# Performance work log

Measured on AMD Instinct MI355X. Metric: run time of the kernel, lower is better.

Reference implementation:

```python
import jax, jax.numpy as jnp
import numpy as np

N = 100000      # nodes
E = 1600000     # directed edges (bidirectional pairs)
DIN = 64
DOUT = 64
T = 3
LMBDA = 0.5
EPS = 1e-9


def setup_inputs() -> dict:
    key = jax.random.key(0)
    k1, k2, k3, k4 = jax.random.split(key, 4)
    x = jax.random.normal(k1, (N, DIN), dtype=jnp.float32)
    Eh = E // 2
    s = jax.random.randint(k2, (Eh,), 0, N)
    d = jax.random.randint(k3, (Eh,), 0, N)
    # bidirectional layout required by assert_bidirectional:
    # row0 = [s, d], row1 = [d, s]
    edge_index = jnp.stack([jnp.concatenate([s, d]), jnp.concatenate([d, s])]).astype(jnp.int32)
    W = jax.random.normal(k4, (DIN, DOUT), dtype=jnp.float32) / np.sqrt(DIN)
    b = jnp.zeros((DOUT,), dtype=jnp.float32)
    lmbda = jnp.float32(LMBDA)
    return {"x": x, "edge_index": edge_index, "W": W, "b": b, "lmbda": lmbda}


def _ema(h, src, dst, lmbda):
    # h: [N, D] node features after linear; src/dst: [E] int
    Eh = src.shape[0] // 2
    deg = jax.ops.segment_sum(jnp.ones(src.shape[0], h.dtype), src, num_segments=N)  # [N]
    h_e = h[src]                       # [E, D]  (expand)
    deg_e = deg[src][:, None]          # [E, 1]
    M = h_e                            # initial edge messages M_ij = x_i
    m = jax.ops.segment_sum(M, dst, num_segments=N)  # [N, D]  (aggregate)
    coef = lmbda / (deg_e - 1.0 + EPS)

    def step(carry, _):
        M, m = carry
        m_e = m[src]                                   # [E, D]
        M_ji = jnp.roll(M, -Eh, axis=0)                # reversed-edge messages
        M_new = jnp.where(deg_e == 1.0, h_e,
                          (1.0 - lmbda) * h_e + coef * (m_e - M_ji))
        m_new = jax.ops.segment_sum(M_new, dst, num_segments=N)
        return (M_new, m_new), None

    (M, m), _ = jax.lax.scan(step, (M, m), None, length=T)
    degN = deg[:, None]
    return jnp.where(degN == 0.0, h,
                     (1.0 - lmbda) * h + lmbda / (degN + EPS) * m)


def reference(x, edge_index, W, b, lmbda):
    src, dst = edge_index[0], edge_index[1]
    x_in = x                       # dim_in == dim_out -> residual uses pre-linear x
    h = x @ W + b                  # pyg_nn.Linear
    y = jax.nn.relu(_ema(h, src, dst, lmbda))
    # dropout p=0.0 (eval) is identity
    return x_in + y
```

## Files before the change

### kernel.cpp

```cpp
#include <hip/hip_runtime.h>
#include <hip/hip_bf16.h>


static __device__ __forceinline__ float bf2f(unsigned short v) {
    union { unsigned int u; float f; } x;
    x.u = ((unsigned int)v) << 16;
    return x.f;
}

static __device__ __forceinline__ unsigned short f2bf(float f) {
    union { unsigned int u; float f; } x;
    x.f = f;
    unsigned int r = x.u + 0x7FFFu + ((x.u >> 16) & 1u);
    return (unsigned short)(r >> 16);
}

static __device__ __forceinline__ float edge_c(int dm1) {
    float fd = (float)dm1;
    float raw = 0.5f * __builtin_amdgcn_rcpf(fd);
    return (fd == 0.0f) ? 0.0f : raw;
}

__global__ void ema_gemm_kernel(const float* __restrict__ x, const float* __restrict__ W,
                                const float* __restrict__ bias, unsigned short* __restrict__ hbf) {
    int wave = (int)((blockIdx.x * 256 + threadIdx.x) >> 6);
    int lane = (int)(threadIdx.x & 63);
    int n0 = wave * 8;
    if (n0 >= 100000) return;
    float w[64];
    #pragma unroll
    for (int k = 0; k < 64; ++k) w[k] = W[k * 64 + lane];
    float bv = bias[lane];
    int nend = (n0 + 8 < 100000) ? (n0 + 8) : 100000;
    for (int n = n0; n < nend; ++n) {
        const float* xr = x + (size_t)__builtin_amdgcn_readfirstlane(n) * 64;
        float acc = bv;
        #pragma unroll
        for (int k = 0; k < 64; ++k) acc = fmaf(xr[k], w[k], acc);
        hbf[n * 64 + lane] = f2bf(acc);
    }
}

__global__ void ema_hist_kernel(const int* ei, int* hcnt) {
    __shared__ int hist[391];
    int t = (int)threadIdx.x;
    int bl = (int)blockIdx.x;
    for (int i = t; i < 391; i += 256) hist[i] = 0;
    __syncthreads();
    int e0 = bl * 4096;
    #pragma unroll
    for (int i = 0; i < 16; ++i) {
        int e = e0 + t + i * 256;
        if (e < 1600000) {
            int dst = (e < 800000) ? ei[e + 800000] : ei[e - 800000];
            atomicAdd(&hist[dst >> 8], 1);
        }
    }
    __syncthreads();
    for (int i = t; i < 391; i += 256) hcnt[i * 391 + bl] = hist[i];
}

__global__ void ema_bscan_row_kernel(int* hcnt, int* btot) {
    __shared__ int s[512];
    int bu = (int)blockIdx.x;
    int t = (int)threadIdx.x;
    int v = (t < 391) ? hcnt[bu * 391 + t] : 0;
    s[t] = v;
    __syncthreads();
    for (int off = 1; off < 512; off <<= 1) {
        int add = (t >= off) ? s[t - off] : 0;
        __syncthreads();
        s[t] += add;
        __syncthreads();
    }
    if (t < 391) hcnt[bu * 391 + t] = s[t] - v;
    if (t == 390) btot[bu] = s[t];
}

__global__ void ema_bscan_base_kernel(const int* btot, int* bbase) {
    __shared__ int s[512];
    int t = (int)threadIdx.x;
    int v = (t < 391) ? btot[t] : 0;
    s[t] = v;
    __syncthreads();
    for (int off = 1; off < 512; off <<= 1) {
        int add = (t >= off) ? s[t - off] : 0;
        __syncthreads();
        s[t] += add;
        __syncthreads();
    }
    if (t < 391) bbase[t] = s[t] - v;
    if (t == 390) bbase[391] = s[t];
}

__global__ void ema_scatter_kernel(const int* ei, const int* hcnt,
                                   const int* bbase, unsigned int* stage) {
    __shared__ int base[391];
    __shared__ int cnt[391];
    int t = (int)threadIdx.x;
    int bl = (int)blockIdx.x;
    for (int i = t; i < 391; i += 256) {
        base[i] = hcnt[i * 391 + bl] + bbase[i];
        cnt[i] = 0;
    }
    __syncthreads();
    int e0 = bl * 4096;
    #pragma unroll
    for (int i = 0; i < 16; ++i) {
        int e = e0 + t + i * 256;
        if (e < 1600000) {
            int src = ei[e];
            int dst = (e < 800000) ? ei[e + 800000] : ei[e - 800000];
            int bu = dst >> 8;
            int slot = base[bu] + atomicAdd(&cnt[bu], 1);
            stage[slot] = ((unsigned int)(dst & 255) << 24) | (unsigned int)src;
        }
    }
}

__global__ void ema_fillcsr_count_kernel(const int* __restrict__ bbase,
                                         const unsigned int* __restrict__ stage,
                                         int* __restrict__ degi,
                                         int* __restrict__ rs) {
    __shared__ int cnt[256];
    __shared__ int scn[256];
    int b = (int)blockIdx.x;
    int t = (int)threadIdx.x;
    cnt[t] = 0;
    __syncthreads();
    int seg_lo = bbase[b];
    int seg_hi = bbase[b + 1];
    for (int i = seg_lo + t; i < seg_hi; i += 256) {
        atomicAdd(&cnt[stage[i] >> 24], 1);
    }
    __syncthreads();
    int v = cnt[t];
    scn[t] = v;
    __syncthreads();
    for (int off = 1; off < 256; off <<= 1) {
        int add = (t >= off) ? scn[t - off] : 0;
        __syncthreads();
        scn[t] += add;
        __syncthreads();
    }
    int node = (b << 8) + t;
    if (node < 100000) {
        degi[node] = v;
        rs[node] = seg_lo + scn[t] - v;
    }
}

__global__ void ema_fillcsr_write_kernel(const int* __restrict__ rs,
                                         const unsigned int* __restrict__ stage,
                                         const int* __restrict__ degi,
                                         int* __restrict__ csr,
                                         float* __restrict__ cf) {
    __shared__ int rsl[256];
    __shared__ int cnt[256];
    int b = (int)blockIdx.x;
    int t = (int)threadIdx.x;
    int node_lo = b << 8;
    int node = node_lo + t;
    rsl[t] = (node < 100000) ? rs[node] : 1600000;
    cnt[t] = 0;
    __syncthreads();
    int seg_lo = rsl[0];
    int seg_hi = (node_lo + 256 < 100000) ? rs[node_lo + 256] : 1600000;
    for (int i = seg_lo + t; i < seg_hi; i += 256) {
        unsigned int v = stage[i];
        int local = (int)(v >> 24);
        int srcn = (int)(v & 0x00FFFFFFu);
        int dm1 = degi[srcn] - 1;
        if (dm1 < 0) dm1 = 0;
        if (dm1 > 32767) dm1 = 32767;
        int slot = rsl[local] + atomicAdd(&cnt[local], 1);
        csr[slot] = (dm1 << 17) | srcn;
        cf[slot] = edge_c(dm1);
    }
}

__global__ void ema_cfcopy_kernel(const float4* __restrict__ cf4,
                                  float4* __restrict__ cfD4) {
    int i = (int)(blockIdx.x * 256 + threadIdx.x);
    if (i < 400000) cfD4[i] = cf4[i];
}

__global__ void ema_passA_kernel(const int* __restrict__ degi, const int* __restrict__ rs,
                                 const int* __restrict__ csr, const float* __restrict__ cf,
                                 const unsigned short* __restrict__ hbf,
                                 unsigned short* __restrict__ m0, unsigned short* __restrict__ W1,
                                 unsigned short* __restrict__ W2, unsigned short* __restrict__ W3a,
                                 float2* __restrict__ pp) {
    int wid = (int)((blockIdx.x * 256 + threadIdx.x) >> 6);
    int c = (int)(threadIdx.x & 63);
    if (wid >= 100000) return;
    int dv = __builtin_amdgcn_readfirstlane(degi[wid]);
    int base = wid * 64 + c;
    float hv = bf2f(hbf[base]);
    if (dv == 0) {
        m0[base] = 0;
        W1[base] = 0;
        W2[base] = 0;
        W3a[base] = f2bf(hv);
        if (c == 0) pp[wid] = make_float2(0.0f, 0.0f);
        return;
    }
    int j = __builtin_amdgcn_readfirstlane(rs[wid]);
    int end = j + dv;
    float av = (dv > 1) ? 0.5f : 1.0f;
    float cv = (dv > 1) ? 0.5f / ((float)dv - 1.0f + 1e-9f) : 0.0f;
    float fv = av * hv;
    float sm = 0.0f, sS = 0.0f, sQ = 0.0f, p1 = 0.0f, p2 = 0.0f;
    for (; j + 4 <= end; j += 4) {
        unsigned int w0 = (unsigned int)csr[j];
        unsigned int w1 = (unsigned int)csr[j + 1];
        unsigned int w2 = (unsigned int)csr[j + 2];
        unsigned int w3 = (unsigned int)csr[j + 3];
        int a0 = (int)(w0 & 0x1FFFFu), d0 = (int)(w0 >> 17);
        int a1 = (int)(w1 & 0x1FFFFu), d1 = (int)(w1 >> 17);
        int a2 = (int)(w2 & 0x1FFFFu), d2 = (int)(w2 >> 17);
        int a3 = (int)(w3 & 0x1FFFFu), d3 = (int)(w3 >> 17);
        float c0 = cf[j], c1 = cf[j + 1], c2 = cf[j + 2], c3 = cf[j + 3];
        float h0 = bf2f(hbf[a0 * 64 + c]);
        float h1 = bf2f(hbf[a1 * 64 + c]);
        float h2 = bf2f(hbf[a2 * 64 + c]);
        float h3 = bf2f(hbf[a3 * 64 + c]);
        float al0 = d0 ? 0.5f : 1.0f;
        float al1 = d1 ? 0.5f : 1.0f;
        float al2 = d2 ? 0.5f : 1.0f;
        float al3 = d3 ? 0.5f : 1.0f;
        sm += (h0 + h1) + (h2 + h3);
        sS += al0 * h0 + al1 * h1 + al2 * h2 + al3 * h3;
        sQ += c0 * h0 + c1 * h1 + c2 * h2 + c3 * h3;
        p1 += (c0 + c1) + (c2 + c3);
        p2 += c0 * c0 + c1 * c1 + c2 * c2 + c3 * c3;
    }
    for (; j < end; ++j) {
        unsigned int w0 = (unsigned int)csr[j];
        int a = (int)(w0 & 0x1FFFFu), d0 = (int)(w0 >> 17);
        float ha = bf2f(hbf[a * 64 + c]);
        float ca = cf[j];
        float ala = d0 ? 0.5f : 1.0f;
        sm += ha;
        sS += ala * ha;
        sQ += ca * ha;
        p1 += ca;
        p2 += ca * ca;
    }
    float r = 0.5f / ((float)dv + 1e-9f);
    float w1o = sS - hv * p1;
    float w2o = sS - fv * p1 - cv * p1 * sm + cv * sQ;
    float w3o = 0.5f * hv + r * (sS - fv * p1 + 0.5f * cv * sQ - cv * hv * p2);
    m0[base] = f2bf(sm);
    W1[base] = f2bf(w1o);
    W2[base] = f2bf(w2o);
    W3a[base] = f2bf(w3o);
    if (c == 0) pp[wid] = make_float2(r * cv * p1, r * cv);
}

__global__ void ema_passB_kernel(const int* __restrict__ degi, const int* __restrict__ rs,
                                 const int* __restrict__ csr, const float* __restrict__ cf,
                                 const unsigned short* __restrict__ m0,
                                 unsigned short* __restrict__ W1m1, unsigned short* __restrict__ W3W4,
                                 const float2* __restrict__ pp) {
    int wid = (int)((blockIdx.x * 256 + threadIdx.x) >> 6);
    int c = (int)(threadIdx.x & 63);
    if (wid >= 100000) return;
    int dv = __builtin_amdgcn_readfirstlane(degi[wid]);
    if (dv == 0) return;
    int base = wid * 64 + c;
    int j = __builtin_amdgcn_readfirstlane(rs[wid]);
    int end = j + dv;
    float t1 = 0.0f, t2 = 0.0f;
    for (; j + 4 <= end; j += 4) {
        unsigned int w0 = (unsigned int)csr[j];
        unsigned int w1 = (unsigned int)csr[j + 1];
        unsigned int w2 = (unsigned int)csr[j + 2];
        unsigned int w3 = (unsigned int)csr[j + 3];
        int a0 = (int)(w0 & 0x1FFFFu);
        int a1 = (int)(w1 & 0x1FFFFu);
        int a2 = (int)(w2 & 0x1FFFFu);
        int a3 = (int)(w3 & 0x1FFFFu);
        float c0 = cf[j], c1 = cf[j + 1], c2 = cf[j + 2], c3 = cf[j + 3];
        float m0v = bf2f(m0[a0 * 64 + c]);
        float m1v = bf2f(m0[a1 * 64 + c]);
        float m2v = bf2f(m0[a2 * 64 + c]);
        float m3v = bf2f(m0[a3 * 64 + c]);
        t1 += c0 * m0v + c1 * m1v + c2 * m2v + c3 * m3v;
        t2 += c0 * c0 * m0v + c1 * c1 * m1v + c2 * c2 * m2v + c3 * c3 * m3v;
    }
    for (; j < end; ++j) {
        unsigned int w0 = (unsigned int)csr[j];
        int a = (int)(w0 & 0x1FFFFu);
        float ca = cf[j];
        float mv = bf2f(m0[a * 64 + c]);
        t1 += ca * mv;
        t2 += ca * ca * mv;
    }
    float2 ppv = pp[wid];
    float m1 = bf2f(W1m1[base]) + t1;
    float w4 = bf2f(W3W4[base]) - ppv.x * m1 + ppv.y * t2;
    W1m1[base] = f2bf(m1);
    W3W4[base] = f2bf(w4);
}

__global__ void ema_passC_kernel(const int* __restrict__ degi, const int* __restrict__ rs,
                                 const int* __restrict__ csr, const float* __restrict__ cf,
                                 const unsigned short* __restrict__ m1,
                                 unsigned short* __restrict__ W2m2) {
    int wid = (int)((blockIdx.x * 256 + threadIdx.x) >> 6);
    int c = (int)(threadIdx.x & 63);
    if (wid >= 100000) return;
    int dv = __builtin_amdgcn_readfirstlane(degi[wid]);
    if (dv == 0) return;
    int base = wid * 64 + c;
    int j = __builtin_amdgcn_readfirstlane(rs[wid]);
    int end = j + dv;
    float t = 0.0f;
    for (; j + 4 <= end; j += 4) {
        unsigned int w0 = (unsigned int)csr[j];
        unsigned int w1 = (unsigned int)csr[j + 1];
        unsigned int w2 = (unsigned int)csr[j + 2];
        unsigned int w3 = (unsigned int)csr[j + 3];
        int a0 = (int)(w0 & 0x1FFFFu);
        int a1 = (int)(w1 & 0x1FFFFu);
        int a2 = (int)(w2 & 0x1FFFFu);
        int a3 = (int)(w3 & 0x1FFFFu);
        float c0 = cf[j], c1 = cf[j + 1], c2 = cf[j + 2], c3 = cf[j + 3];
        float m0v = bf2f(m1[a0 * 64 + c]);
        float m1v = bf2f(m1[a1 * 64 + c]);
        float m2v = bf2f(m1[a2 * 64 + c]);
        float m3v = bf2f(m1[a3 * 64 + c]);
        t += c0 * m0v + c1 * m1v + c2 * m2v + c3 * m3v;
    }
    for (; j < end; ++j) {
        unsigned int w0 = (unsigned int)csr[j];
        int a = (int)(w0 & 0x1FFFFu);
        t += cf[j] * bf2f(m1[a * 64 + c]);
    }
    float m2v = bf2f(W2m2[base]) + t;
    W2m2[base] = f2bf(m2v);
}

__global__ void GraphEMALayer_18133351924067_kernel(
    const int* __restrict__ degi, const int* __restrict__ rs,
    const int* __restrict__ csr, const float* __restrict__ cfD,
    const unsigned short* __restrict__ m2, const unsigned short* __restrict__ W4,
    const float* __restrict__ x, float* __restrict__ out) {
    int wid = (int)((blockIdx.x * 256 + threadIdx.x) >> 6);
    int c = (int)(threadIdx.x & 63);
    if (wid >= 100000) return;
    int dv = __builtin_amdgcn_readfirstlane(degi[wid]);
    int base = wid * 64 + c;
    float xv = x[base];
    float y = bf2f(W4[base]);
    if (dv > 0) {
        int j = __builtin_amdgcn_readfirstlane(rs[wid]);
        int end = j + dv;
        float t = 0.0f;
        for (; j + 4 <= end; j += 4) {
            unsigned int w0 = (unsigned int)csr[j];
            unsigned int w1 = (unsigned int)csr[j + 1];
            unsigned int w2 = (unsigned int)csr[j + 2];
            unsigned int w3 = (unsigned int)csr[j + 3];
            int a0 = (int)(w0 & 0x1FFFFu);
            int a1 = (int)(w1 & 0x1FFFFu);
            int a2 = (int)(w2 & 0x1FFFFu);
            int a3 = (int)(w3 & 0x1FFFFu);
            float c0 = cfD[j], c1 = cfD[j + 1], c2 = cfD[j + 2], c3 = cfD[j + 3];
            float m0v = bf2f(m2[a0 * 64 + c]);
            float m1v = bf2f(m2[a1 * 64 + c]);
            float m2v = bf2f(m2[a2 * 64 + c]);
            float m3v = bf2f(m2[a3 * 64 + c]);
            t += c0 * m0v + c1 * m1v + c2 * m2v + c3 * m3v;
        }
        for (; j < end; ++j) {
            unsigned int w0 = (unsigned int)csr[j];
            int a = (int)(w0 & 0x1FFFFu);
            t += cfD[j] * bf2f(m2[a * 64 + c]);
        }
        float r = 0.5f / ((float)dv + 1e-9f);
        y += r * t;
    }
    if (y < 0.0f) y = 0.0f;
    out[base] = xv + y;
}

extern "C" void kernel_launch(void* const* d_in, const int* in_sizes, int n_in,
                              void* d_out, int out_size, void* d_ws, size_t ws_size,
                              hipStream_t stream) {
    (void)in_sizes; (void)n_in; (void)out_size; (void)ws_size;

    const float* x    = (const float*)d_in[0];
    const int*   ei   = (const int*)d_in[1];
    const float* W    = (const float*)d_in[2];
    const float* bias = (const float*)d_in[3];
    float* out = (float*)d_out;
    unsigned short* m0 = (unsigned short*)d_out;
    float* cf = (float*)((char*)d_out + 12800000);

    char* ws = (char*)d_ws;
    unsigned short* hbf  = (unsigned short*)(ws);
    unsigned short* W1m1 = (unsigned short*)(ws + 12800000);
    unsigned short* W2m2 = (unsigned short*)(ws + 25600000);
    unsigned short* W3W4 = (unsigned short*)(ws + 38400000);
    int* degi = (int*)(ws + 51200000);
    int* rs   = (int*)(ws + 51600000);
    float2* pp   = (float2*)(ws + 52800000);
    int* csr  = (int*)(ws + 53600000);
    int* bbase = (int*)(ws + 60000000);
    int* btot  = (int*)(ws + 60002048);

    unsigned int* stage = (unsigned int*)(ws + 12800000);
    int* hcnt = (int*)(ws + 25600000);
    float* cfD = (float*)(ws);

    int eb = (100000 * 64 + 255) / 256;
    int nb = (100000 + 255) / 256;
    int pb = (1600000 + 4095) / 4096;
    int gb = (100000 + 31) / 32;
    int cb = (400000 + 255) / 256;

    ema_gemm_kernel<<<gb, 256, 0, stream>>>(x, W, bias, hbf);

    ema_hist_kernel<<<pb, 256, 0, stream>>>(ei, hcnt);
    ema_bscan_row_kernel<<<391, 512, 0, stream>>>(hcnt, btot);
    ema_bscan_base_kernel<<<1, 512, 0, stream>>>(btot, bbase);
    ema_scatter_kernel<<<pb, 256, 0, stream>>>(ei, hcnt, bbase, stage);
    ema_fillcsr_count_kernel<<<nb, 256, 0, stream>>>(bbase, stage, degi, rs);
    ema_fillcsr_write_kernel<<<nb, 256, 0, stream>>>(rs, stage, degi, csr, cf);

    ema_passA_kernel<<<eb, 256, 0, stream>>>(degi, rs, csr, cf, hbf,
                                             m0, W1m1, W2m2, W3W4, pp);
    ema_cfcopy_kernel<<<cb, 256, 0, stream>>>((const float4*)cf, (float4*)cfD);
    ema_passB_kernel<<<eb, 256, 0, stream>>>(degi, rs, csr, cf, m0,
                                             W1m1, W3W4, pp);
    ema_passC_kernel<<<eb, 256, 0, stream>>>(degi, rs, csr, cf, W1m1, W2m2);
    GraphEMALayer_18133351924067_kernel<<<eb, 256, 0, stream>>>(
        degi, rs, csr, cfD, W2m2, W3W4, x, out);
}
```

Baseline: 387.3 us.

## Process neighbor pairs per wave with packed bf16x2 loads; merge CSR fill kernels

The four gather passes now split each wave into two 32-lane halves. Each half handles one neighbor of a pair and loads two bf16 features per lane as a 32-bit word. The halves are combined at the end with a cross-half shuffle. This halves per-edge gather instructions and loop trips on degree-bounded latency chains, at the cost of an extra reduction and idle lanes on odd tails. The CSR count and write kernels are merged into one. The coefficient array is generated in a separate elementwise kernel, and the degree is no longer packed into the CSR index; a zero-coefficient test replaces that degree-one check.

```diff
diff --git a/kernel.cpp b/kernel.cpp
--- a/kernel.cpp
+++ b/kernel.cpp
@@ -13,6 +13,20 @@
     x.f = f;
     unsigned int r = x.u + 0x7FFFu + ((x.u >> 16) & 1u);
     return (unsigned short)(r >> 16);
+}
+
+static __device__ __forceinline__ float bflo(unsigned int u) {
+    union { unsigned int u; float f; } x;
+    x.u = u << 16;
+    return x.f;
+}
+static __device__ __forceinline__ float bfhi(unsigned int u) {
+    union { unsigned int u; float f; } x;
+    x.u = u & 0xFFFF0000u;
+    return x.f;
+}
+static __device__ __forceinline__ unsigned int pack2bf(float lo, float hi) {
+    return (unsigned int)f2bf(lo) | ((unsigned int)f2bf(hi) << 16);
 }
 
 static __device__ __forceinline__ float edge_c(int dm1) {
@@ -118,12 +132,14 @@
     }
 }
 
-__global__ void ema_fillcsr_count_kernel(const int* __restrict__ bbase,
-                                         const unsigned int* __restrict__ stage,
-                                         int* __restrict__ degi,
-                                         int* __restrict__ rs) {
+__global__ void ema_fillcsr_kernel(const int* __restrict__ bbase,
+                                   const unsigned int* __restrict__ stage,
+                                   int* __restrict__ degi,
+                                   int* __restrict__ rs,
+                                   int* __restrict__ csr) {
     __shared__ int cnt[256];
     __shared__ int scn[256];
+    __shared__ int rsl[256];
     int b = (int)blockIdx.x;
     int t = (int)threadIdx.x;
     cnt[t] = 0;
@@ -143,40 +159,30 @@
         scn[t] += add;
         __syncthreads();
     }
+    int start = seg_lo + scn[t] - v;
+    rsl[t] = start;
     int node = (b << 8) + t;
     if (node < 100000) {
         degi[node] = v;
-        rs[node] = seg_lo + scn[t] - v;
-    }
-}
-
-__global__ void ema_fillcsr_write_kernel(const int* __restrict__ rs,
-                                         const unsigned int* __restrict__ stage,
-                                         const int* __restrict__ degi,
-                                         int* __restrict__ csr,
-                                         float* __restrict__ cf) {
-    __shared__ int rsl[256];
-    __shared__ int cnt[256];
-    int b = (int)blockIdx.x;
-    int t = (int)threadIdx.x;
-    int node_lo = b << 8;
-    int node = node_lo + t;
-    rsl[t] = (node < 100000) ? rs[node] : 1600000;
+        rs[node] = start;
+    }
     cnt[t] = 0;
     __syncthreads();
-    int seg_lo = rsl[0];
-    int seg_hi = (node_lo + 256 < 100000) ? rs[node_lo + 256] : 1600000;
     for (int i = seg_lo + t; i < seg_hi; i += 256) {
-        unsigned int v = stage[i];
-        int local = (int)(v >> 24);
-        int srcn = (int)(v & 0x00FFFFFFu);
-        int dm1 = degi[srcn] - 1;
-        if (dm1 < 0) dm1 = 0;
-        if (dm1 > 32767) dm1 = 32767;
+        unsigned int s = stage[i];
+        int local = (int)(s >> 24);
+        int srcn = (int)(s & 0x00FFFFFFu);
         int slot = rsl[local] + atomicAdd(&cnt[local], 1);
-        csr[slot] = (dm1 << 17) | srcn;
-        cf[slot] = edge_c(dm1);
-    }
+        csr[slot] = srcn;
+    }
+}
+
+__global__ void ema_cfgen_kernel(const int* __restrict__ csr,
+                                 const int* __restrict__ degi,
+                                 float* __restrict__ cf) {
+    int i = (int)(blockIdx.x * 256 + threadIdx.x);
+    if (i >= 1600000) return;
+    cf[i] = edge_c(degi[csr[i]] - 1);
 }
 
 __global__ void ema_cfcopy_kernel(const float4* __restrict__ cf4,
@@ -187,203 +193,296 @@
 
 __global__ void ema_passA_kernel(const int* __restrict__ degi, const int* __restrict__ rs,
                                  const int* __restrict__ csr, const float* __restrict__ cf,
-                                 const unsigned short* __restrict__ hbf,
-                                 unsigned short* __restrict__ m0, unsigned short* __restrict__ W1,
-                                 unsigned short* __restrict__ W2, unsigned short* __restrict__ W3a,
+                                 const unsigned int* __restrict__ hb32,
+                                 unsigned int* __restrict__ m0, unsigned int* __restrict__ W1,
+                                 unsigned int* __restrict__ W2, unsigned int* __restrict__ W3a,
                                  float2* __restrict__ pp) {
     int wid = (int)((blockIdx.x * 256 + threadIdx.x) >> 6);
-    int c = (int)(threadIdx.x & 63);
+    int lane = (int)(threadIdx.x & 63);
     if (wid >= 100000) return;
+    int half = lane >> 5;
+    int k = lane & 31;
     int dv = __builtin_amdgcn_readfirstlane(degi[wid]);
-    int base = wid * 64 + c;
-    float hv = bf2f(hbf[base]);
+    int own = wid * 32 + k;
+    unsigned int hown = hb32[own];
+    float hlo = bflo(hown), hhi = bfhi(hown);
     if (dv == 0) {
-        m0[base] = 0;
-        W1[base] = 0;
-        W2[base] = 0;
-        W3a[base] = f2bf(hv);
-        if (c == 0) pp[wid] = make_float2(0.0f, 0.0f);
+        if (half == 0) {
+            m0[own] = 0u;
+            W1[own] = 0u;
+            W2[own] = 0u;
+            W3a[own] = pack2bf(hlo, hhi);
+        }
+        if (lane == 0) pp[wid] = make_float2(0.0f, 0.0f);
         return;
     }
     int j = __builtin_amdgcn_readfirstlane(rs[wid]);
-    int end = j + dv;
     float av = (dv > 1) ? 0.5f : 1.0f;
     float cv = (dv > 1) ? 0.5f / ((float)dv - 1.0f + 1e-9f) : 0.0f;
-    float fv = av * hv;
-    float sm = 0.0f, sS = 0.0f, sQ = 0.0f, p1 = 0.0f, p2 = 0.0f;
-    for (; j + 4 <= end; j += 4) {
-        unsigned int w0 = (unsigned int)csr[j];
-        unsigned int w1 = (unsigned int)csr[j + 1];
-        unsigned int w2 = (unsigned int)csr[j + 2];
-        unsigned int w3 = (unsigned int)csr[j + 3];
-        int a0 = (int)(w0 & 0x1FFFFu), d0 = (int)(w0 >> 17);
-        int a1 = (int)(w1 & 0x1FFFFu), d1 = (int)(w1 >> 17);
-        int a2 = (int)(w2 & 0x1FFFFu), d2 = (int)(w2 >> 17);
-        int a3 = (int)(w3 & 0x1FFFFu), d3 = (int)(w3 >> 17);
-        float c0 = cf[j], c1 = cf[j + 1], c2 = cf[j + 2], c3 = cf[j + 3];
-        float h0 = bf2f(hbf[a0 * 64 + c]);
-        float h1 = bf2f(hbf[a1 * 64 + c]);
-        float h2 = bf2f(hbf[a2 * 64 + c]);
-        float h3 = bf2f(hbf[a3 * 64 + c]);
-        float al0 = d0 ? 0.5f : 1.0f;
-        float al1 = d1 ? 0.5f : 1.0f;
-        float al2 = d2 ? 0.5f : 1.0f;
-        float al3 = d3 ? 0.5f : 1.0f;
-        sm += (h0 + h1) + (h2 + h3);
-        sS += al0 * h0 + al1 * h1 + al2 * h2 + al3 * h3;
-        sQ += c0 * h0 + c1 * h1 + c2 * h2 + c3 * h3;
-        p1 += (c0 + c1) + (c2 + c3);
-        p2 += c0 * c0 + c1 * c1 + c2 * c2 + c3 * c3;
-    }
-    for (; j < end; ++j) {
-        unsigned int w0 = (unsigned int)csr[j];
-        int a = (int)(w0 & 0x1FFFFu), d0 = (int)(w0 >> 17);
-        float ha = bf2f(hbf[a * 64 + c]);
-        float ca = cf[j];
-        float ala = d0 ? 0.5f : 1.0f;
-        sm += ha;
-        sS += ala * ha;
-        sQ += ca * ha;
-        p1 += ca;
-        p2 += ca * ca;
-    }
+    float smL = 0.0f, smH = 0.0f, sQL = 0.0f, sQH = 0.0f;
+    float sLL = 0.0f, sLH = 0.0f, p1 = 0.0f, p2 = 0.0f;
+    int npair = dv >> 1;
+    int p = 0;
+    for (; p + 8 <= npair; p += 8) {
+        int e = j + (p << 1);
+        #pragma unroll
+        for (int u = 0; u < 8; ++u) {
+            int a0 = csr[e + 2 * u], a1 = csr[e + 2 * u + 1];
+            float c0 = cf[e + 2 * u], c1 = cf[e + 2 * u + 1];
+            int asel = half ? a1 : a0;
+            float ce = half ? c1 : c0;
+            unsigned int uu = hb32[asel * 32 + k];
+            float vlo = bflo(uu), vhi = bfhi(uu);
+            smL += vlo; smH += vhi;
+            sQL = fmaf(ce, vlo, sQL); sQH = fmaf(ce, vhi, sQH);
+            p1 += ce; p2 = fmaf(ce, ce, p2);
+            if (__float_as_uint(c0) == 0u || __float_as_uint(c1) == 0u) {
+                if (ce == 0.0f) { sLL += vlo; sLH += vhi; }
+            }
+        }
+    }
+    for (; p < npair; ++p) {
+        int e = j + (p << 1);
+        int a0 = csr[e], a1 = csr[e + 1];
+        float c0 = cf[e], c1 = cf[e + 1];
+        int asel = half ? a1 : a0;
+        float ce = half ? c1 : c0;
+        unsigned int uu = hb32[asel * 32 + k];
+        float vlo = bflo(uu), vhi = bfhi(uu);
+        smL += vlo; smH += vhi;
+        sQL = fmaf(ce, vlo, sQL); sQH = fmaf(ce, vhi, sQH);
+        p1 += ce; p2 = fmaf(ce, ce, p2);
+        if (__float_as_uint(c0) == 0u || __float_as_uint(c1) == 0u) {
+            if (ce == 0.0f) { sLL += vlo; sLH += vhi; }
+        }
+    }
+    if (dv & 1) {
+        int e = j + dv - 1;
+        int a = csr[e];
+        float c0 = cf[e];
+        if (half == 0) {
+            unsigned int uu = hb32[a * 32 + k];
+            float vlo = bflo(uu), vhi = bfhi(uu);
+            smL += vlo; smH += vhi;
+            sQL = fmaf(c0, vlo, sQL); sQH = fmaf(c0, vhi, sQH);
+            p1 += c0; p2 = fmaf(c0, c0, p2);
+            if (__float_as_uint(c0) == 0u) { sLL += vlo; sLH += vhi; }
+        }
+    }
+    smL += __shfl_xor(smL, 32); smH += __shfl_xor(smH, 32);
+    sQL += __shfl_xor(sQL, 32); sQH += __shfl_xor(sQH, 32);
+    sLL += __shfl_xor(sLL, 32); sLH += __shfl_xor(sLH, 32);
+    p1  += __shfl_xor(p1, 32);  p2  += __shfl_xor(p2, 32);
+    float sSL = 0.5f * (smL + sLL), sSH = 0.5f * (smH + sLH);
     float r = 0.5f / ((float)dv + 1e-9f);
-    float w1o = sS - hv * p1;
-    float w2o = sS - fv * p1 - cv * p1 * sm + cv * sQ;
-    float w3o = 0.5f * hv + r * (sS - fv * p1 + 0.5f * cv * sQ - cv * hv * p2);
-    m0[base] = f2bf(sm);
-    W1[base] = f2bf(w1o);
-    W2[base] = f2bf(w2o);
-    W3a[base] = f2bf(w3o);
-    if (c == 0) pp[wid] = make_float2(r * cv * p1, r * cv);
+    float fvL = av * hlo, fvH = av * hhi;
+    float w1L = sSL - hlo * p1;
+    float w1H = sSH - hhi * p1;
+    float w2L = sSL - fvL * p1 - cv * p1 * smL + cv * sQL;
+    float w2H = sSH - fvH * p1 - cv * p1 * smH + cv * sQH;
+    float w3L = 0.5f * hlo + r * (sSL - fvL * p1 + 0.5f * cv * sQL - cv * hlo * p2);
+    float w3H = 0.5f * hhi + r * (sSH - fvH * p1 + 0.5f * cv * sQH - cv * hhi * p2);
+    if (half == 0) {
+        m0[own]  = pack2bf(smL, smH);
+        W1[own]  = pack2bf(w1L, w1H);
+        W2[own]  = pack2bf(w2L, w2H);
+        W3a[own] = pack2bf(w3L, w3H);
+    }
+    if (lane == 0) pp[wid] = make_float2(r * cv * p1, r * cv);
 }
 
 __global__ void ema_passB_kernel(const int* __restrict__ degi, const int* __restrict__ rs,
                                  const int* __restrict__ csr, const float* __restrict__ cf,
-                                 const unsigned short* __restrict__ m0,
-                                 unsigned short* __restrict__ W1m1, unsigned short* __restrict__ W3W4,
+                                 const unsigned int* __restrict__ m032,
+                                 unsigned int* __restrict__ W1m1, unsigned int* __restrict__ W3W4,
                                  const float2* __restrict__ pp) {
     int wid = (int)((blockIdx.x * 256 + threadIdx.x) >> 6);
-    int c = (int)(threadIdx.x & 63);
+    int lane = (int)(threadIdx.x & 63);
     if (wid >= 100000) return;
     int dv = __builtin_amdgcn_readfirstlane(degi[wid]);
     if (dv == 0) return;
-    int base = wid * 64 + c;
+    int half = lane >> 5;
+    int k = lane & 31;
     int j = __builtin_amdgcn_readfirstlane(rs[wid]);
-    int end = j + dv;
-    float t1 = 0.0f, t2 = 0.0f;
-    for (; j + 4 <= end; j += 4) {
-        unsigned int w0 = (unsigned int)csr[j];
-        unsigned int w1 = (unsigned int)csr[j + 1];
-        unsigned int w2 = (unsigned int)csr[j + 2];
-        unsigned int w3 = (unsigned int)csr[j + 3];
-        int a0 = (int)(w0 & 0x1FFFFu);
-        int a1 = (int)(w1 & 0x1FFFFu);
-        int a2 = (int)(w2 & 0x1FFFFu);
-        int a3 = (int)(w3 & 0x1FFFFu);
-        float c0 = cf[j], c1 = cf[j + 1], c2 = cf[j + 2], c3 = cf[j + 3];
-        float m0v = bf2f(m0[a0 * 64 + c]);
-        float m1v = bf2f(m0[a1 * 64 + c]);
-        float m2v = bf2f(m0[a2 * 64 + c]);
-        float m3v = bf2f(m0[a3 * 64 + c]);
-        t1 += c0 * m0v + c1 * m1v + c2 * m2v + c3 * m3v;
-        t2 += c0 * c0 * m0v + c1 * c1 * m1v + c2 * c2 * m2v + c3 * c3 * m3v;
-    }
-    for (; j < end; ++j) {
-        unsigned int w0 = (unsigned int)csr[j];
-        int a = (int)(w0 & 0x1FFFFu);
-        float ca = cf[j];
-        float mv = bf2f(m0[a * 64 + c]);
-        t1 += ca * mv;
-        t2 += ca * ca * mv;
-    }
+    float t1L = 0.0f, t1H = 0.0f, t2L = 0.0f, t2H = 0.0f;
+    int npair = dv >> 1;
+    int p = 0;
+    for (; p + 8 <= npair; p += 8) {
+        int e = j + (p << 1);
+        #pragma unroll
+        for (int u = 0; u < 8; ++u) {
+            int a0 = csr[e + 2 * u], a1 = csr[e + 2 * u + 1];
+            float c0 = cf[e + 2 * u], c1 = cf[e + 2 * u + 1];
+            int asel = half ? a1 : a0;
+            float ce = half ? c1 : c0;
+            unsigned int uu = m032[asel * 32 + k];
+            float vlo = bflo(uu), vhi = bfhi(uu);
+            float ce2 = ce * ce;
+            t1L = fmaf(ce, vlo, t1L); t1H = fmaf(ce, vhi, t1H);
+            t2L = fmaf(ce2, vlo, t2L); t2H = fmaf(ce2, vhi, t2H);
+        }
+    }
+    for (; p < npair; ++p) {
+        int e = j + (p << 1);
+        int a0 = csr[e], a1 = csr[e + 1];
+        float c0 = cf[e], c1 = cf[e + 1];
+        int asel = half ? a1 : a0;
+        float ce = half ? c1 : c0;
+        unsigned int uu = m032[asel * 32 + k];
+        float vlo = bflo(uu), vhi = bfhi(uu);
+        float ce2 = ce * ce;
+        t1L = fmaf(ce, vlo, t1L); t1H = fmaf(ce, vhi, t1H);
+        t2L = fmaf(ce2, vlo, t2L); t2H = fmaf(ce2, vhi, t2H);
+    }
+    if (dv & 1) {
+        int e = j + dv - 1;
+        int a = csr[e];
+        float c0 = cf[e];
+        if (half == 0) {
+            unsigned int uu = m032[a * 32 + k];
+            float vlo = bflo(uu), vhi = bfhi(uu);
+            float c02 = c0 * c0;
+            t1L = fmaf(c0, vlo, t1L); t1H = fmaf(c0, vhi, t1H);
+            t2L = fmaf(c02, vlo, t2L); t2H = fmaf(c02, vhi, t2H);
+        }
+    }
+    t1L += __shfl_xor(t1L, 32); t1H += __shfl_xor(t1H, 32);
+    t2L += __shfl_xor(t2L, 32); t2H += __shfl_xor(t2H, 32);
+    int own = wid * 32 + k;
+    unsigned int w1own = W1m1[own];
+    unsigned int w3own = W3W4[own];
     float2 ppv = pp[wid];
-    float m1 = bf2f(W1m1[base]) + t1;
-    float w4 = bf2f(W3W4[base]) - ppv.x * m1 + ppv.y * t2;
-    W1m1[base] = f2bf(m1);
-    W3W4[base] = f2bf(w4);
+    float m1L = bflo(w1own) + t1L;
+    float m1H = bfhi(w1own) + t1H;
+    float w4L = bflo(w3own) - ppv.x * m1L + ppv.y * t2L;
+    float w4H = bfhi(w3own) - ppv.x * m1H + ppv.y * t2H;
+    if (half == 0) {
+        W1m1[own] = pack2bf(m1L, m1H);
+        W3W4[own] = pack2bf(w4L, w4H);
+    }
 }
 
 __global__ void ema_passC_kernel(const int* __restrict__ degi, const int* __restrict__ rs,
                                  const int* __restrict__ csr, const float* __restrict__ cf,
-                                 const unsigned short* __restrict__ m1,
-                                 unsigned short* __restrict__ W2m2) {
+                                 const unsigned int* __restrict__ m132,
+                                 unsigned int* __restrict__ W2m2) {
     int wid = (int)((blockIdx.x * 256 + threadIdx.x) >> 6);
-    int c = (int)(threadIdx.x & 63);
+    int lane = (int)(threadIdx.x & 63);
     if (wid >= 100000) return;
     int dv = __builtin_amdgcn_readfirstlane(degi[wid]);
     if (dv == 0) return;
-    int base = wid * 64 + c;
+    int half = lane >> 5;
+    int k = lane & 31;
     int j = __builtin_amdgcn_readfirstlane(rs[wid]);
-    int end = j + dv;
-    float t = 0.0f;
-    for (; j + 4 <= end; j += 4) {
-        unsigned int w0 = (unsigned int)csr[j];
-        unsigned int w1 = (unsigned int)csr[j + 1];
-        unsigned int w2 = (unsigned int)csr[j + 2];
-        unsigned int w3 = (unsigned int)csr[j + 3];
-        int a0 = (int)(w0 & 0x1FFFFu);
-        int a1 = (int)(w1 & 0x1FFFFu);
-        int a2 = (int)(w2 & 0x1FFFFu);
-        int a3 = (int)(w3 & 0x1FFFFu);
-        float c0 = cf[j], c1 = cf[j + 1], c2 = cf[j + 2], c3 = cf[j + 3];
-        float m0v = bf2f(m1[a0 * 64 + c]);
-        float m1v = bf2f(m1[a1 * 64 + c]);
-        float m2v = bf2f(m1[a2 * 64 + c]);
-        float m3v = bf2f(m1[a3 * 64 + c]);
-        t += c0 * m0v + c1 * m1v + c2 * m2v + c3 * m3v;
-    }
-    for (; j < end; ++j) {
-        unsigned int w0 = (unsigned int)csr[j];
-        int a = (int)(w0 & 0x1FFFFu);
-        t += cf[j] * bf2f(m1[a * 64 + c]);
-    }
-    float m2v = bf2f(W2m2[base]) + t;
-    W2m2[base] = f2bf(m2v);
+    float tL = 0.0f, tH = 0.0f;
+    int npair = dv >> 1;
+    int p = 0;
+    for (; p + 8 <= npair; p += 8) {
+        int e = j + (p << 1);
+        #pragma unroll
+        for (int u = 0; u < 8; ++u) {
+            int a0 = csr[e + 2 * u], a1 = csr[e + 2 * u + 1];
+            float c0 = cf[e + 2 * u], c1 = cf[e + 2 * u + 1];
+            int asel = half ? a1 : a0;
+            float ce = half ? c1 : c0;
+            unsigned int uu = m132[asel * 32 + k];
+            tL = fmaf(ce, bflo(uu), tL);
+            tH = fmaf(ce, bfhi(uu), tH);
+        }
+    }
+    for (; p < npair; ++p) {
+        int e = j + (p << 1);
+        int a0 = csr[e], a1 = csr[e + 1];
+        float c0 = cf[e], c1 = cf[e + 1];
+        int asel = half ? a1 : a0;
+        float ce = half ? c1 : c0;
+        unsigned int uu = m132[asel * 32 + k];
+        tL = fmaf(ce, bflo(uu), tL);
+        tH = fmaf(ce, bfhi(uu), tH);
+    }
+    if (dv & 1) {
+        int e = j + dv - 1;
+        int a = csr[e];
+        float c0 = cf[e];
+        if (half == 0) {
+            unsigned int uu = m132[a * 32 + k];
+            tL = fmaf(c0, bflo(uu), tL);
+            tH = fmaf(c0, bfhi(uu), tH);
+        }
+    }
+    tL += __shfl_xor(tL, 32);
+    tH += __shfl_xor(tH, 32);
+    int own = wid * 32 + k;
+    unsigned int w2own = W2m2[own];
+    if (half == 0) {
+        W2m2[own] = pack2bf(bflo(w2own) + tL, bfhi(w2own) + tH);
+    }
 }
 
 __global__ void GraphEMALayer_18133351924067_kernel(
     const int* __restrict__ degi, const int* __restrict__ rs,
     const int* __restrict__ csr, const float* __restrict__ cfD,
-    const unsigned short* __restrict__ m2, const unsigned short* __restrict__ W4,
-    const float* __restrict__ x, float* __restrict__ out) {
+    const unsigned int* __restrict__ m232, const unsigned int* __restrict__ W4,
+    const float2* __restrict__ x2, float2* __restrict__ out2) {
     int wid = (int)((blockIdx.x * 256 + threadIdx.x) >> 6);
-    int c = (int)(threadIdx.x & 63);
+    int lane = (int)(threadIdx.x & 63);
     if (wid >= 100000) return;
+    int half = lane >> 5;
+    int k = lane & 31;
     int dv = __builtin_amdgcn_readfirstlane(degi[wid]);
-    int base = wid * 64 + c;
-    float xv = x[base];
-    float y = bf2f(W4[base]);
+    int own = wid * 32 + k;
+    float2 xv = x2[own];
+    unsigned int w4own = W4[own];
+    float yL = bflo(w4own), yH = bfhi(w4own);
     if (dv > 0) {
         int j = __builtin_amdgcn_readfirstlane(rs[wid]);
-        int end = j + dv;
-        float t = 0.0f;
-        for (; j + 4 <= end; j += 4) {
-            unsigned int w0 = (unsigned int)csr[j];
-            unsigned int w1 = (unsigned int)csr[j + 1];
-            unsigned int w2 = (unsigned int)csr[j + 2];
-            unsigned int w3 = (unsigned int)csr[j + 3];
-            int a0 = (int)(w0 & 0x1FFFFu);
-            int a1 = (int)(w1 & 0x1FFFFu);
-            int a2 = (int)(w2 & 0x1FFFFu);
-            int a3 = (int)(w3 & 0x1FFFFu);
-            float c0 = cfD[j], c1 = cfD[j + 1], c2 = cfD[j + 2], c3 = cfD[j + 3];
-            float m0v = bf2f(m2[a0 * 64 + c]);
-            float m1v = bf2f(m2[a1 * 64 + c]);
-            float m2v = bf2f(m2[a2 * 64 + c]);
-            float m3v = bf2f(m2[a3 * 64 + c]);
-            t += c0 * m0v + c1 * m1v + c2 * m2v + c3 * m3v;
-        }
-        for (; j < end; ++j) {
-            unsigned int w0 = (unsigned int)csr[j];
-            int a = (int)(w0 & 0x1FFFFu);
-            t += cfD[j] * bf2f(m2[a * 64 + c]);
-        }
+        float tL = 0.0f, tH = 0.0f;
+        int npair = dv >> 1;
+        int p = 0;
+        for (; p + 8 <= npair; p += 8) {
+            int e = j + (p << 1);
+            #pragma unroll
+            for (int u = 0; u < 8; ++u) {
+                int a0 = csr[e + 2 * u], a1 = csr[e + 2 * u + 1];
+                float c0 = cfD[e + 2 * u], c1 = cfD[e + 2 * u + 1];
+                int asel = half ? a1 : a0;
+                float ce = half ? c1 : c0;
+                unsigned int uu = m232[asel * 32 + k];
+                tL = fmaf(ce, bflo(uu), tL);
+                tH = fmaf(ce, bfhi(uu), tH);
+            }
+        }
+        for (; p < npair; ++p) {
+            int e = j + (p << 1);
+            int a0 = csr[e], a1 = csr[e + 1];
+            float c0 = cfD[e], c1 = cfD[e + 1];
+            int asel = half ? a1 : a0;
+            float ce = half ? c1 : c0;
+            unsigned int uu = m232[asel * 32 + k];
+            tL = fmaf(ce, bflo(uu), tL);
+            tH = fmaf(ce, bfhi(uu), tH);
+        }
+        if (dv & 1) {
+            int e = j + dv - 1;
+            int a = csr[e];
+            float c0 = cfD[e];
+            if (half == 0) {
+                unsigned int uu = m232[a * 32 + k];
+                tL = fmaf(c0, bflo(uu), tL);
+                tH = fmaf(c0, bfhi(uu), tH);
+            }
+        }
+        tL += __shfl_xor(tL, 32);
+        tH += __shfl_xor(tH, 32);
         float r = 0.5f / ((float)dv + 1e-9f);
-        y += r * t;
-    }
-    if (y < 0.0f) y = 0.0f;
-    out[base] = xv + y;
+        yL += r * tL;
+        yH += r * tH;
+    }
+    if (yL < 0.0f) yL = 0.0f;
+    if (yH < 0.0f) yH = 0.0f;
+    if (half == 0) {
+        out2[own] = make_float2(xv.x + yL, xv.y + yH);
+    }
 }
 
 extern "C" void kernel_launch(void* const* d_in, const int* in_sizes, int n_in,
@@ -395,18 +494,17 @@
     const int*   ei   = (const int*)d_in[1];
     const float* W    = (const float*)d_in[2];
     const float* bias = (const float*)d_in[3];
-    float* out = (float*)d_out;
-    unsigned short* m0 = (unsigned short*)d_out;
-    float* cf = (float*)((char*)d_out + 12800000);
+    unsigned int* m0 = (unsigned int*)d_out;
+    float* cf  = (float*)((char*)d_out + 12800000);
 
     char* ws = (char*)d_ws;
     unsigned short* hbf  = (unsigned short*)(ws);
-    unsigned short* W1m1 = (unsigned short*)(ws + 12800000);
-    unsigned short* W2m2 = (unsigned short*)(ws + 25600000);
-    unsigned short* W3W4 = (unsigned short*)(ws + 38400000);
+    unsigned int* W1m1 = (unsigned int*)(ws + 12800000);
+    unsigned int* W2m2 = (unsigned int*)(ws + 25600000);
+    unsigned int* W3W4 = (unsigned int*)(ws + 38400000);
     int* degi = (int*)(ws + 51200000);
     int* rs   = (int*)(ws + 51600000);
-    float2* pp   = (float2*)(ws + 52800000);
+    float2* pp  = (float2*)(ws + 52800000);
     int* csr  = (int*)(ws + 53600000);
     int* bbase = (int*)(ws + 60000000);
     int* btot  = (int*)(ws + 60002048);
@@ -419,6 +517,7 @@
     int nb = (100000 + 255) / 256;
     int pb = (1600000 + 4095) / 4096;
     int gb = (100000 + 31) / 32;
+    int db = (1600000 + 255) / 256;
     int cb = (400000 + 255) / 256;
 
     ema_gemm_kernel<<<gb, 256, 0, stream>>>(x, W, bias, hbf);
@@ -427,15 +526,17 @@
     ema_bscan_row_kernel<<<391, 512, 0, stream>>>(hcnt, btot);
     ema_bscan_base_kernel<<<1, 512, 0, stream>>>(btot, bbase);
     ema_scatter_kernel<<<pb, 256, 0, stream>>>(ei, hcnt, bbase, stage);
-    ema_fillcsr_count_kernel<<<nb, 256, 0, stream>>>(bbase, stage, degi, rs);
-    ema_fillcsr_write_kernel<<<nb, 256, 0, stream>>>(rs, stage, degi, csr, cf);
-
-    ema_passA_kernel<<<eb, 256, 0, stream>>>(degi, rs, csr, cf, hbf,
+    ema_fillcsr_kernel<<<nb, 256, 0, stream>>>(bbase, stage, degi, rs, csr);
+    ema_cfgen_kernel<<<db, 256, 0, stream>>>(csr, degi, cf);
+
+    ema_passA_kernel<<<eb, 256, 0, stream>>>(degi, rs, csr, cf,
+                                             (const unsigned int*)hbf,
                                              m0, W1m1, W2m2, W3W4, pp);
     ema_cfcopy_kernel<<<cb, 256, 0, stream>>>((const float4*)cf, (float4*)cfD);
     ema_passB_kernel<<<eb, 256, 0, stream>>>(degi, rs, csr, cf, m0,
                                              W1m1, W3W4, pp);
     ema_passC_kernel<<<eb, 256, 0, stream>>>(degi, rs, csr, cf, W1m1, W2m2);
     GraphEMALayer_18133351924067_kernel<<<eb, 256, 0, stream>>>(
-        degi, rs, csr, cfD, W2m2, W3W4, x, out);
-}
+        degi, rs, csr, cfD, W2m2, W3W4,
+        (const float2*)x, (float2*)d_out);
+}
```

Measured after the change: 395.5 us. 1.02x slower.

## Merge CSR count/write kernels, split coefficient generation, unroll gathers by 16

Applied to the files above, without the earlier changes.

Fuses the CSR count and write kernels into one block-local pass and moves coefficient computation into a separate per-edge kernel. Neighbour degree is no longer packed into the CSR word; the alpha term is now derived from cf==0. The gather loops in all passes are unrolled 16-wide, issuing all index and feature loads before accumulating, to give more memory-level parallelism. This raises register pressure, adds one extra launch, and changes FP rounding slightly through fmaf.

```diff
diff --git a/kernel.cpp b/kernel.cpp
--- a/kernel.cpp
+++ b/kernel.cpp
@@ -118,12 +118,14 @@
     }
 }
 
-__global__ void ema_fillcsr_count_kernel(const int* __restrict__ bbase,
-                                         const unsigned int* __restrict__ stage,
-                                         int* __restrict__ degi,
-                                         int* __restrict__ rs) {
+__global__ void ema_fillcsr_kernel(const int* __restrict__ bbase,
+                                   const unsigned int* __restrict__ stage,
+                                   int* __restrict__ degi,
+                                   int* __restrict__ rs,
+                                   int* __restrict__ csr) {
     __shared__ int cnt[256];
     __shared__ int scn[256];
+    __shared__ int rsl[256];
     int b = (int)blockIdx.x;
     int t = (int)threadIdx.x;
     cnt[t] = 0;
@@ -143,40 +145,30 @@
         scn[t] += add;
         __syncthreads();
     }
+    int start = seg_lo + scn[t] - v;
+    rsl[t] = start;
     int node = (b << 8) + t;
     if (node < 100000) {
         degi[node] = v;
-        rs[node] = seg_lo + scn[t] - v;
-    }
-}
-
-__global__ void ema_fillcsr_write_kernel(const int* __restrict__ rs,
-                                         const unsigned int* __restrict__ stage,
-                                         const int* __restrict__ degi,
-                                         int* __restrict__ csr,
-                                         float* __restrict__ cf) {
-    __shared__ int rsl[256];
-    __shared__ int cnt[256];
-    int b = (int)blockIdx.x;
-    int t = (int)threadIdx.x;
-    int node_lo = b << 8;
-    int node = node_lo + t;
-    rsl[t] = (node < 100000) ? rs[node] : 1600000;
+        rs[node] = start;
+    }
     cnt[t] = 0;
     __syncthreads();
-    int seg_lo = rsl[0];
-    int seg_hi = (node_lo + 256 < 100000) ? rs[node_lo + 256] : 1600000;
     for (int i = seg_lo + t; i < seg_hi; i += 256) {
-        unsigned int v = stage[i];
-        int local = (int)(v >> 24);
-        int srcn = (int)(v & 0x00FFFFFFu);
-        int dm1 = degi[srcn] - 1;
-        if (dm1 < 0) dm1 = 0;
-        if (dm1 > 32767) dm1 = 32767;
+        unsigned int s = stage[i];
+        int local = (int)(s >> 24);
+        int srcn = (int)(s & 0x00FFFFFFu);
         int slot = rsl[local] + atomicAdd(&cnt[local], 1);
-        csr[slot] = (dm1 << 17) | srcn;
-        cf[slot] = edge_c(dm1);
-    }
+        csr[slot] = srcn;
+    }
+}
+
+__global__ void ema_cfgen_kernel(const int* __restrict__ csr,
+                                 const int* __restrict__ degi,
+                                 float* __restrict__ cf) {
+    int i = (int)(blockIdx.x * 256 + threadIdx.x);
+    if (i >= 1600000) return;
+    cf[i] = edge_c(degi[csr[i]] - 1);
 }
 
 __global__ void ema_cfcopy_kernel(const float4* __restrict__ cf4,
@@ -211,41 +203,52 @@
     float cv = (dv > 1) ? 0.5f / ((float)dv - 1.0f + 1e-9f) : 0.0f;
     float fv = av * hv;
     float sm = 0.0f, sS = 0.0f, sQ = 0.0f, p1 = 0.0f, p2 = 0.0f;
+    for (; j + 16 <= end; j += 16) {
+        int aa[16];
+        float cc[16];
+        float hh[16];
+        #pragma unroll
+        for (int u = 0; u < 16; ++u) { aa[u] = csr[j + u]; cc[u] = cf[j + u]; }
+        #pragma unroll
+        for (int u = 0; u < 16; ++u) { hh[u] = bf2f(hbf[aa[u] * 64 + c]); }
+        #pragma unroll
+        for (int u = 0; u < 16; ++u) {
+            float al = (cc[u] == 0.0f) ? 1.0f : 0.5f;
+            sm += hh[u];
+            sS = fmaf(al, hh[u], sS);
+            sQ = fmaf(cc[u], hh[u], sQ);
+            p1 += cc[u];
+            p2 = fmaf(cc[u], cc[u], p2);
+        }
+    }
     for (; j + 4 <= end; j += 4) {
-        unsigned int w0 = (unsigned int)csr[j];
-        unsigned int w1 = (unsigned int)csr[j + 1];
-        unsigned int w2 = (unsigned int)csr[j + 2];
-        unsigned int w3 = (unsigned int)csr[j + 3];
-        int a0 = (int)(w0 & 0x1FFFFu), d0 = (int)(w0 >> 17);
-        int a1 = (int)(w1 & 0x1FFFFu), d1 = (int)(w1 >> 17);
-        int a2 = (int)(w2 & 0x1FFFFu), d2 = (int)(w2 >> 17);
-        int a3 = (int)(w3 & 0x1FFFFu), d3 = (int)(w3 >> 17);
-        float c0 = cf[j], c1 = cf[j + 1], c2 = cf[j + 2], c3 = cf[j + 3];
-        float h0 = bf2f(hbf[a0 * 64 + c]);
-        float h1 = bf2f(hbf[a1 * 64 + c]);
-        float h2 = bf2f(hbf[a2 * 64 + c]);
-        float h3 = bf2f(hbf[a3 * 64 + c]);
-        float al0 = d0 ? 0.5f : 1.0f;
-        float al1 = d1 ? 0.5f : 1.0f;
-        float al2 = d2 ? 0.5f : 1.0f;
-        float al3 = d3 ? 0.5f : 1.0f;
-        sm += (h0 + h1) + (h2 + h3);
-        sS += al0 * h0 + al1 * h1 + al2 * h2 + al3 * h3;
-        sQ += c0 * h0 + c1 * h1 + c2 * h2 + c3 * h3;
-        p1 += (c0 + c1) + (c2 + c3);
-        p2 += c0 * c0 + c1 * c1 + c2 * c2 + c3 * c3;
+        int aa[4];
+        float cc[4];
+        float hh[4];
+        #pragma unroll
+        for (int u = 0; u < 4; ++u) { aa[u] = csr[j + u]; cc[u] = cf[j + u]; }
+        #pragma unroll
+        for (int u = 0; u < 4; ++u) { hh[u] = bf2f(hbf[aa[u] * 64 + c]); }
+        #pragma unroll
+        for (int u = 0; u < 4; ++u) {
+            float al = (cc[u] == 0.0f) ? 1.0f : 0.5f;
+            sm += hh[u];
+            sS = fmaf(al, hh[u], sS);
+            sQ = fmaf(cc[u], hh[u], sQ);
+            p1 += cc[u];
+            p2 = fmaf(cc[u], cc[u], p2);
+        }
     }
     for (; j < end; ++j) {
-        unsigned int w0 = (unsigned int)csr[j];
-        int a = (int)(w0 & 0x1FFFFu), d0 = (int)(w0 >> 17);
+        int a = csr[j];
+        float ca = cf[j];
         float ha = bf2f(hbf[a * 64 + c]);
-        float ca = cf[j];
-        float ala = d0 ? 0.5f : 1.0f;
+        float al = (ca == 0.0f) ? 1.0f : 0.5f;
         sm += ha;
-        sS += ala * ha;
-        sQ += ca * ha;
+        sS = fmaf(al, ha, sS);
+        sQ = fmaf(ca, ha, sQ);
         p1 += ca;
-        p2 += ca * ca;
+        p2 = fmaf(ca, ca, p2);
     }
     float r = 0.5f / ((float)dv + 1e-9f);
     float w1o = sS - hv * p1;
@@ -272,30 +275,39 @@
     int j = __builtin_amdgcn_readfirstlane(rs[wid]);
     int end = j + dv;
     float t1 = 0.0f, t2 = 0.0f;
+    for (; j + 16 <= end; j += 16) {
+        int aa[16];
+        float cc[16];
+        float vv[16];
+        #pragma unroll
+        for (int u = 0; u < 16; ++u) { aa[u] = csr[j + u]; cc[u] = cf[j + u]; }
+        #pragma unroll
+        for (int u = 0; u < 16; ++u) { vv[u] = bf2f(m0[aa[u] * 64 + c]); }
+        #pragma unroll
+        for (int u = 0; u < 16; ++u) {
+            t1 = fmaf(cc[u], vv[u], t1);
+            t2 = fmaf(cc[u] * cc[u], vv[u], t2);
+        }
+    }
     for (; j + 4 <= end; j += 4) {
-        unsigned int w0 = (unsigned int)csr[j];
-        unsigned int w1 = (unsigned int)csr[j + 1];
-        unsigned int w2 = (unsigned int)csr[j + 2];
-        unsigned int w3 = (unsigned int)csr[j + 3];
-        int a0 = (int)(w0 & 0x1FFFFu);
-        int a1 = (int)(w1 & 0x1FFFFu);
-        int a2 = (int)(w2 & 0x1FFFFu);
-        int a3 = (int)(w3 & 0x1FFFFu);
-        float c0 = cf[j], c1 = cf[j + 1], c2 = cf[j + 2], c3 = cf[j + 3];
-        float m0v = bf2f(m0[a0 * 64 + c]);
-        float m1v = bf2f(m0[a1 * 64 + c]);
-        float m2v = bf2f(m0[a2 * 64 + c]);
-        float m3v = bf2f(m0[a3 * 64 + c]);
-        t1 += c0 * m0v + c1 * m1v + c2 * m2v + c3 * m3v;
-        t2 += c0 * c0 * m0v + c1 * c1 * m1v + c2 * c2 * m2v + c3 * c3 * m3v;
+        int aa[4];
+        float cc[4];
+        float vv[4];
+        #pragma unroll
+        for (int u = 0; u < 4; ++u) { aa[u] = csr[j + u]; cc[u] = cf[j + u]; }
+        #pragma unroll
+        for (int u = 0; u < 4; ++u) { vv[u] = bf2f(m0[aa[u] * 64 + c]); }
+        #pragma unroll
+        for (int u = 0; u < 4; ++u) {
+            t1 = fmaf(cc[u], vv[u], t1);
+            t2 = fmaf(cc[u] * cc[u], vv[u], t2);
+        }
     }
     for (; j < end; ++j) {
-        unsigned int w0 = (unsigned int)csr[j];
-        int a = (int)(w0 & 0x1FFFFu);
         float ca = cf[j];
-        float mv = bf2f(m0[a * 64 + c]);
-        t1 += ca * mv;
-        t2 += ca * ca * mv;
+        float mv = bf2f(m0[csr[j] * 64 + c]);
+        t1 = fmaf(ca, mv, t1);
+        t2 = fmaf(ca * ca, mv, t2);
     }
     float2 ppv = pp[wid];
     float m1 = bf2f(W1m1[base]) + t1;
@@ -317,26 +329,30 @@
     int j = __builtin_amdgcn_readfirstlane(rs[wid]);
     int end = j + dv;
     float t = 0.0f;
+    for (; j + 16 <= end; j += 16) {
+        int aa[16];
+        float cc[16];
+        float vv[16];
+        #pragma unroll
+        for (int u = 0; u < 16; ++u) { aa[u] = csr[j + u]; cc[u] = cf[j + u]; }
+        #pragma unroll
+        for (int u = 0; u < 16; ++u) { vv[u] = bf2f(m1[aa[u] * 64 + c]); }
+        #pragma unroll
+        for (int u = 0; u < 16; ++u) { t = fmaf(cc[u], vv[u], t); }
+    }
     for (; j + 4 <= end; j += 4) {
-        unsigned int w0 = (unsigned int)csr[j];
-        unsigned int w1 = (unsigned int)csr[j + 1];
-        unsigned int w2 = (unsigned int)csr[j + 2];
-        unsigned int w3 = (unsigned int)csr[j + 3];
-        int a0 = (int)(w0 & 0x1FFFFu);
-        int a1 = (int)(w1 & 0x1FFFFu);
-        int a2 = (int)(w2 & 0x1FFFFu);
-        int a3 = (int)(w3 & 0x1FFFFu);
-        float c0 = cf[j], c1 = cf[j + 1], c2 = cf[j + 2], c3 = cf[j + 3];
-        float m0v = bf2f(m1[a0 * 64 + c]);
-        float m1v = bf2f(m1[a1 * 64 + c]);
-        float m2v = bf2f(m1[a2 * 64 + c]);
-        float m3v = bf2f(m1[a3 * 64 + c]);
-        t += c0 * m0v + c1 * m1v + c2 * m2v + c3 * m3v;
+        int aa[4];
+        float cc[4];
+        float vv[4];
+        #pragma unroll
+        for (int u = 0; u < 4; ++u) { aa[u] = csr[j + u]; cc[u] = cf[j + u]; }
+        #pragma unroll
+        for (int u = 0; u < 4; ++u) { vv[u] = bf2f(m1[aa[u] * 64 + c]); }
+        #pragma unroll
+        for (int u = 0; u < 4; ++u) { t = fmaf(cc[u], vv[u], t); }
     }
     for (; j < end; ++j) {
-        unsigned int w0 = (unsigned int)csr[j];
-        int a = (int)(w0 & 0x1FFFFu);
-        t += cf[j] * bf2f(m1[a * 64 + c]);
+        t = fmaf(cf[j], bf2f(m1[csr[j] * 64 + c]), t);
     }
     float m2v = bf2f(W2m2[base]) + t;
     W2m2[base] = f2bf(m2v);
@@ -358,26 +374,30 @@
         int j = __builtin_amdgcn_readfirstlane(rs[wid]);
         int end = j + dv;
         float t = 0.0f;
+        for (; j + 16 <= end; j += 16) {
+            int aa[16];
+            float cc[16];
+            float vv[16];
+            #pragma unroll
+            for (int u = 0; u < 16; ++u) { aa[u] = csr[j + u]; cc[u] = cfD[j + u]; }
+            #pragma unroll
+            for (int u = 0; u < 16; ++u) { vv[u] = bf2f(m2[aa[u] * 64 + c]); }
+            #pragma unroll
+            for (int u = 0; u < 16; ++u) { t = fmaf(cc[u], vv[u], t); }
+        }
         for (; j + 4 <= end; j += 4) {
-            unsigned int w0 = (unsigned int)csr[j];
-            unsigned int w1 = (unsigned int)csr[j + 1];
-            unsigned int w2 = (unsigned int)csr[j + 2];
-            unsigned int w3 = (unsigned int)csr[j + 3];
-            int a0 = (int)(w0 & 0x1FFFFu);
-            int a1 = (int)(w1 & 0x1FFFFu);
-            int a2 = (int)(w2 & 0x1FFFFu);
-            int a3 = (int)(w3 & 0x1FFFFu);
-            float c0 = cfD[j], c1 = cfD[j + 1], c2 = cfD[j + 2], c3 = cfD[j + 3];
-            float m0v = bf2f(m2[a0 * 64 + c]);
-            float m1v = bf2f(m2[a1 * 64 + c]);
-            float m2v = bf2f(m2[a2 * 64 + c]);
-            float m3v = bf2f(m2[a3 * 64 + c]);
-            t += c0 * m0v + c1 * m1v + c2 * m2v + c3 * m3v;
+            int aa[4];
+            float cc[4];
+            float vv[4];
+            #pragma unroll
+            for (int u = 0; u < 4; ++u) { aa[u] = csr[j + u]; cc[u] = cfD[j + u]; }
+            #pragma unroll
+            for (int u = 0; u < 4; ++u) { vv[u] = bf2f(m2[aa[u] * 64 + c]); }
+            #pragma unroll
+            for (int u = 0; u < 4; ++u) { t = fmaf(cc[u], vv[u], t); }
         }
         for (; j < end; ++j) {
-            unsigned int w0 = (unsigned int)csr[j];
-            int a = (int)(w0 & 0x1FFFFu);
-            t += cfD[j] * bf2f(m2[a * 64 + c]);
+            t = fmaf(cfD[j], bf2f(m2[csr[j] * 64 + c]), t);
         }
         float r = 0.5f / ((float)dv + 1e-9f);
         y += r * t;
@@ -397,7 +417,7 @@
     const float* bias = (const float*)d_in[3];
     float* out = (float*)d_out;
     unsigned short* m0 = (unsigned short*)d_out;
-    float* cf = (float*)((char*)d_out + 12800000);
+    float* cf  = (float*)((char*)d_out + 12800000);
 
     char* ws = (char*)d_ws;
     unsigned short* hbf  = (unsigned short*)(ws);
@@ -406,7 +426,7 @@
     unsigned short* W3W4 = (unsigned short*)(ws + 38400000);
     int* degi = (int*)(ws + 51200000);
     int* rs   = (int*)(ws + 51600000);
-    float2* pp   = (float2*)(ws + 52800000);
+    float2* pp  = (float2*)(ws + 52800000);
     int* csr  = (int*)(ws + 53600000);
     int* bbase = (int*)(ws + 60000000);
     int* btot  = (int*)(ws + 60002048);
@@ -419,6 +439,7 @@
     int nb = (100000 + 255) / 256;
     int pb = (1600000 + 4095) / 4096;
     int gb = (100000 + 31) / 32;
+    int db = (1600000 + 255) / 256;
     int cb = (400000 + 255) / 256;
 
     ema_gemm_kernel<<<gb, 256, 0, stream>>>(x, W, bias, hbf);
@@ -427,8 +448,8 @@
     ema_bscan_row_kernel<<<391, 512, 0, stream>>>(hcnt, btot);
     ema_bscan_base_kernel<<<1, 512, 0, stream>>>(btot, bbase);
     ema_scatter_kernel<<<pb, 256, 0, stream>>>(ei, hcnt, bbase, stage);
-    ema_fillcsr_count_kernel<<<nb, 256, 0, stream>>>(bbase, stage, degi, rs);
-    ema_fillcsr_write_kernel<<<nb, 256, 0, stream>>>(rs, stage, degi, csr, cf);
+    ema_fillcsr_kernel<<<nb, 256, 0, stream>>>(bbase, stage, degi, rs, csr);
+    ema_cfgen_kernel<<<db, 256, 0, stream>>>(csr, degi, cf);
 
     ema_passA_kernel<<<eb, 256, 0, stream>>>(degi, rs, csr, cf, hbf,
                                              m0, W1m1, W2m2, W3W4, pp);
```

Result: faster. 360.1 us (-7.0%).
